# Optimization experiments

Measured on AMD Instinct MI355X. Metric: run time of the kernel, lower is better.

## Reference

```python
import jax, jax.numpy as jnp
import numpy as np

# Emformer config (from torchaudio.models.Emformer in BasicNet4)
D, H, FFN, L = 512, 4, 128, 4      # input_dim, num_heads, ffn_dim, num_layers
SEG, RC = 4, 1                     # segment_length, right_context_length
B, T = 8, 1025
U = T - RC                         # utterance length = 1024
NSEG = -(-U // SEG)                # 256 segments
R = NSEG * RC                      # total right-context frames = 256
DH = D // H


def _right_context_indices():
    # torchaudio _gen_right_context: segment i's right context = frames [(i+1)*SEG : (i+1)*SEG+RC],
    # last block = input[T-RC:]
    idx = [np.arange((i + 1) * SEG, (i + 1) * SEG + RC) for i in range(NSEG - 1)]
    idx.append(np.arange(T - RC, T))
    return np.concatenate(idx)


def _attention_mask():
    # Rows / cols ordered [right-context blocks (seg order), utterance frames].
    # A query belonging to segment i may attend to segment i's right-context block
    # and segment i's utterance frames (left_context_length=0, no memory bank).
    seg_rc = np.repeat(np.arange(NSEG), RC)
    seg_u = np.arange(U) // SEG
    seg_q = np.concatenate([seg_rc, seg_u])
    seg_k = np.concatenate([seg_rc, seg_u])
    return seg_q[:, None] == seg_k[None, :]  # (R+U, R+U), True = allowed


def _ln(x, g, b, eps=1e-5):
    mu = jnp.mean(x, -1, keepdims=True)
    var = jnp.mean(jnp.square(x - mu), -1, keepdims=True)
    return (x - mu) * jax.lax.rsqrt(var + eps) * g + b


def setup_inputs() -> dict:
    key = jax.random.key(0)
    ks = jax.random.split(key, 8)
    s = 0.02
    return {
        "x": jax.random.normal(ks[0], (B, T, D), jnp.float32),
        "Wq": jax.random.normal(ks[1], (L, D, D), jnp.float32) * s,
        "bq": jnp.zeros((L, D), jnp.float32),
        "Wkv": jax.random.normal(ks[2], (L, 2 * D, D), jnp.float32) * s,
        "bkv": jnp.zeros((L, 2 * D), jnp.float32),
        "Wo": jax.random.normal(ks[3], (L, D, D), jnp.float32) * s,
        "bo": jnp.zeros((L, D), jnp.float32),
        "W1": jax.random.normal(ks[4], (L, FFN, D), jnp.float32) * s,
        "b1": jnp.zeros((L, FFN), jnp.float32),
        "W2": jax.random.normal(ks[5], (L, D, FFN), jnp.float32) * s,
        "b2": jnp.zeros((L, D), jnp.float32),
        "ln_in_g": jnp.ones((L, D), jnp.float32),
        "ln_in_b": jnp.zeros((L, D), jnp.float32),
        "ff_ln_g": jnp.ones((L, D), jnp.float32),
        "ff_ln_b": jnp.zeros((L, D), jnp.float32),
        "ln_out_g": jnp.ones((L, D), jnp.float32),
        "ln_out_b": jnp.zeros((L, D), jnp.float32),
    }


def reference(x, Wq, bq, Wkv, bkv, Wo, bo, W1, b1, W2, b2,
              ln_in_g, ln_in_b, ff_ln_g, ff_ln_b, ln_out_g, ln_out_b):
    rc_idx = jnp.asarray(_right_context_indices())
    allowed = jnp.asarray(_attention_mask())
    scale = DH ** -0.5
    u = x[:, :U]          # (B, U, D) utterance
    r = x[:, rc_idx]      # (B, R, D) gathered right-context blocks
    for l in range(L):
        cat = jnp.concatenate([r, u], axis=1)            # (B, R+U, D)
        ln = _ln(cat, ln_in_g[l], ln_in_b[l])            # pre-attention LN
        q = (ln @ Wq[l].T + bq[l]).reshape(B, R + U, H, DH)
        kv = ln @ Wkv[l].T + bkv[l]
        k = kv[..., :D].reshape(B, R + U, H, DH)
        v = kv[..., D:].reshape(B, R + U, H, DH)
        scores = jnp.einsum("bqhd,bkhd->bhqk", q * scale, k)
        scores = jnp.where(allowed, scores, -jnp.inf)
        probs = jax.nn.softmax(scores, axis=-1)
        attn = jnp.einsum("bhqk,bkhd->bqhd", probs, v).reshape(B, R + U, D)
        rc_out = attn @ Wo[l].T + bo[l] + cat            # residual w/ pre-LN input
        h = _ln(rc_out, ff_ln_g[l], ff_ln_b[l])
        h = jax.nn.relu(h @ W1[l].T + b1[l]) @ W2[l].T + b2[l]
        rc_out = _ln(rc_out + h, ln_out_g[l], ln_out_b[l])
        r, u = rc_out[:, :R], rc_out[:, R:]
    return u.mean(axis=1)  # (B, D): mean-pool over utterance frames
```

## Files before the change

### kernel.cpp

```cpp
#include <hip/hip_runtime.h>
#include <cstdint>
#include <cstddef>

#define D_    512
#define H_    4
#define DH_   128
#define FFN_  128
#define L_    4
#define B_    8
#define T_    1025
#define U_    1024
#define NSEG_ 256
#define R_    256
#define TOT_  1280
#define M_    (B_*TOT_)
#define CH_   1536

typedef __attribute__((ext_vector_type(8))) short bf16x8;
typedef __attribute__((ext_vector_type(4))) float f32x4;
typedef unsigned short u16;

__device__ __forceinline__ u16 f2bf(float f) {
  unsigned u = __builtin_bit_cast(unsigned, f);
  u += 0x7fff + ((u >> 16) & 1);
  return (u16)(u >> 16);
}
__device__ __forceinline__ float bf2f(u16 h) {
  unsigned u = ((unsigned)h) << 16;
  return __builtin_bit_cast(float, u);
}

__device__ __forceinline__ void gload_lds16(const void* g, void* l) {
  __builtin_amdgcn_global_load_lds(
      (const __attribute__((address_space(1))) unsigned*)g,
      (__attribute__((address_space(3))) unsigned*)l, 16, 0, 0);
}

__global__ __launch_bounds__(256)
void cvt_all_k(const float* __restrict__ Wq, const float* __restrict__ Wkv,
               const float* __restrict__ Wo, const float* __restrict__ W1,
               const float* __restrict__ W2, const float* __restrict__ bq,
               const float* __restrict__ bkv,
               u16* __restrict__ WQKVb, u16* __restrict__ Wob,
               u16* __restrict__ W1b, u16* __restrict__ W2b,
               float* __restrict__ bQKV) {
  int i4 = blockIdx.x * 256 + threadIdx.x;
  if (i4 < 786432) {
    int e = i4 * 4;
    int l = e / 786432;
    int rem = e - l * 786432;
    int n = rem >> 9, k = rem & 511;
    const float* src = (n < 512) ? (Wq + (size_t)l * 262144 + n * 512 + k)
                                 : (Wkv + (size_t)l * 524288 + (n - 512) * 512 + k);
    float4 v = *(const float4*)src;
    ushort4 o; o.x = f2bf(v.x); o.y = f2bf(v.y); o.z = f2bf(v.z); o.w = f2bf(v.w);
    *(ushort4*)(WQKVb + e) = o;
  } else if (i4 < 1048576) {
    int e = (i4 - 786432) * 4;
    float4 v = *(const float4*)(Wo + e);
    ushort4 o; o.x = f2bf(v.x); o.y = f2bf(v.y); o.z = f2bf(v.z); o.w = f2bf(v.w);
    *(ushort4*)(Wob + e) = o;
  } else if (i4 < 1114112) {
    int e = (i4 - 1048576) * 4;
    float4 v = *(const float4*)(W1 + e);
    ushort4 o; o.x = f2bf(v.x); o.y = f2bf(v.y); o.z = f2bf(v.z); o.w = f2bf(v.w);
    *(ushort4*)(W1b + e) = o;
  } else if (i4 < 1179648) {
    int e = (i4 - 1114112) * 4;
    float4 v = *(const float4*)(W2 + e);
    ushort4 o; o.x = f2bf(v.x); o.y = f2bf(v.y); o.z = f2bf(v.z); o.w = f2bf(v.w);
    *(ushort4*)(W2b + e) = o;
  } else if (i4 < 1181184) {
    int e = (i4 - 1179648) * 4;
    int l = e / 1536, n = e - l * 1536;
#pragma unroll
    for (int t = 0; t < 4; ++t) {
      int nn = n + t;
      bQKV[e + t] = (nn < 512) ? bq[l * 512 + nn] : bkv[l * 1024 + (nn - 512)];
    }
  }
}

__global__ __launch_bounds__(256)
void gather_ln_k(const float* __restrict__ x, const float* __restrict__ g,
                 const float* __restrict__ bb, float* __restrict__ X,
                 u16* __restrict__ LNb) {
  int row = blockIdx.x;
  int tid = threadIdx.x;
  int b = row / TOT_, p = row % TOT_;
  int t = (p < R_) ? ((p < R_ - 1) ? 4 * (p + 1) : (T_ - 1)) : (p - R_);
  const float* xr = x + ((size_t)b * T_ + t) * D_;
  float e0 = xr[tid], e1 = xr[tid + 256];
  X[(size_t)row * D_ + tid] = e0;
  X[(size_t)row * D_ + tid + 256] = e1;
  float s = e0 + e1, ss = e0 * e0 + e1 * e1;
#pragma unroll
  for (int off = 32; off > 0; off >>= 1) {
    s  += __shfl_down(s, off);
    ss += __shfl_down(ss, off);
  }
  __shared__ float red[10];
  int wid = tid >> 6, lane = tid & 63;
  if (lane == 0) { red[wid] = s; red[4 + wid] = ss; }
  __syncthreads();
  if (tid == 0) {
    float S = red[0] + red[1] + red[2] + red[3];
    float SS = red[4] + red[5] + red[6] + red[7];
    float mu = S * (1.0f / D_);
    float var = SS * (1.0f / D_) - mu * mu;
    if (var < 0.f) var = 0.f;
    red[8] = mu; red[9] = rsqrtf(var + 1e-5f);
  }
  __syncthreads();
  float mu = red[8], rs = red[9];
  u16* yr = LNb + (size_t)row * D_;
  yr[tid]       = f2bf((e0 - mu) * rs * g[tid]       + bb[tid]);
  yr[tid + 256] = f2bf((e1 - mu) * rs * g[tid + 256] + bb[tid + 256]);
}

#define GBM 128
#define GBN 128
#define GBK 32

__global__ __launch_bounds__(256)
void gemm_qkv(const u16* __restrict__ A, const u16* __restrict__ Bw,
              const float* __restrict__ bias, u16* __restrict__ Cout,
              int M, int N, int K) {
  __shared__ __align__(16) u16 As[GBM * GBK];
  __shared__ __align__(16) u16 Bs[GBN * GBK];
  const int tid = threadIdx.x;
  const int wid = tid >> 6;
  const int lane = tid & 63;
  const int bm = blockIdx.y * GBM;
  const int bn = blockIdx.x * GBN;
  const int wr = wid >> 1, wc = wid & 1;

  const int srow = tid >> 2;
  const int skoff = (tid & 3) << 3;

  f32x4 acc[4][4] = {};

  const u16* Ag0 = A  + (size_t)(bm + srow)      * K + skoff;
  const u16* Ag1 = A  + (size_t)(bm + 64 + srow) * K + skoff;
  const u16* Bg0 = Bw + (size_t)(bn + srow)      * K + skoff;
  const u16* Bg1 = Bw + (size_t)(bn + 64 + srow) * K + skoff;
  u16* AsW0 = &As[(size_t)(wid * 16)      * GBK];
  u16* AsW1 = &As[(size_t)(64 + wid * 16) * GBK];
  u16* BsW0 = &Bs[(size_t)(wid * 16)      * GBK];
  u16* BsW1 = &Bs[(size_t)(64 + wid * 16) * GBK];

  const int lrow = lane & 15;
  const int lko  = (lane >> 4) * 16;

  for (int k0 = 0; k0 < K; k0 += GBK) {
    __syncthreads();
    gload_lds16(Ag0 + k0, AsW0);
    gload_lds16(Ag1 + k0, AsW1);
    gload_lds16(Bg0 + k0, BsW0);
    gload_lds16(Bg1 + k0, BsW1);
    __syncthreads();

    bf16x8 afrag[4], bfrag[4];
#pragma unroll
    for (int m = 0; m < 4; ++m) {
      int row = wr * 64 + m * 16 + lrow;
      afrag[m] = *(const bf16x8*)((const char*)As + row * (GBK * 2) + lko);
    }
#pragma unroll
    for (int n = 0; n < 4; ++n) {
      int col = wc * 64 + n * 16 + lrow;
      bfrag[n] = *(const bf16x8*)((const char*)Bs + col * (GBK * 2) + lko);
    }
#pragma unroll
    for (int m = 0; m < 4; ++m)
#pragma unroll
      for (int n = 0; n < 4; ++n)
        acc[m][n] = __builtin_amdgcn_mfma_f32_16x16x32_bf16(
            afrag[m], bfrag[n], acc[m][n], 0, 0, 0);
  }

  const int lcol  = lane & 15;
  const int lrow4 = (lane >> 4) * 4;
#pragma unroll
  for (int m = 0; m < 4; ++m) {
    int rowbase = bm + wr * 64 + m * 16 + lrow4;
#pragma unroll
    for (int n = 0; n < 4; ++n) {
      int col = bn + wc * 64 + n * 16 + lcol;
      float bv = bias[col];
#pragma unroll
      for (int j = 0; j < 4; ++j) {
        int row = rowbase + j;
        ((u16*)Cout)[(size_t)row * N + col] = f2bf(acc[m][n][j] + bv);
      }
    }
  }
}

template <int MODE>
__global__ __launch_bounds__(256)
void gemm_row_ln(const u16* __restrict__ A, const u16* __restrict__ Bw,
                 const float* __restrict__ bias, const float* __restrict__ Rsd,
                 float* __restrict__ Xout,
                 const float* __restrict__ g1, const float* __restrict__ b1,
                 const float* __restrict__ g2, const float* __restrict__ b2,
                 u16* __restrict__ OutBf, int K) {
  __shared__ __align__(16) u16 As[32 * 32];
  __shared__ __align__(16) u16 Bs[512 * 32];
  __shared__ float wsum[4][32], wss[4][32], mu_s[32], rs_s[32];
  const int tid = threadIdx.x;
  const int wid = tid >> 6, lane = tid & 63;
  const int bm = blockIdx.x * 32;
  const int l4 = lane >> 2;
  const int k8 = (lane & 3) << 3;
  const int lrow = lane & 15;
  const int lko  = (lane >> 4) * 16;

  f32x4 acc[2][8] = {};

  const u16* Ag = A + (size_t)(bm + (wid & 1) * 16 + l4) * K + k8;

  for (int k0 = 0; k0 < K; k0 += 32) {
    __syncthreads();
    if (wid < 2)
      gload_lds16(Ag + k0, (char*)As + (wid * 16) * 64);
#pragma unroll
    for (int p = 0; p < 8; ++p) {
      int row = wid * 128 + p * 16 + l4;
      gload_lds16(Bw + (size_t)row * K + k0 + k8,
                  (char*)Bs + (wid * 128 + p * 16) * 64);
    }
    __syncthreads();

    bf16x8 af[2], bf[8];
#pragma unroll
    for (int m = 0; m < 2; ++m)
      af[m] = *(const bf16x8*)((const char*)As + (m * 16 + lrow) * 64 + lko);
#pragma unroll
    for (int n = 0; n < 8; ++n)
      bf[n] = *(const bf16x8*)((const char*)Bs + (wid * 128 + n * 16 + lrow) * 64 + lko);
#pragma unroll
    for (int m = 0; m < 2; ++m)
#pragma unroll
      for (int n = 0; n < 8; ++n)
        acc[m][n] = __builtin_amdgcn_mfma_f32_16x16x32_bf16(
            af[m], bf[n], acc[m][n], 0, 0, 0);
  }

  const int lcol = lane & 15;
  const int lr4 = (lane >> 4) * 4;
#pragma unroll
  for (int n = 0; n < 8; ++n) {
    int col = wid * 128 + n * 16 + lcol;
    float bv = bias[col];
#pragma unroll
    for (int m = 0; m < 2; ++m)
#pragma unroll
      for (int j = 0; j < 4; ++j) {
        int row = bm + m * 16 + lr4 + j;
        float t = acc[m][n][j] + bv + Rsd[(size_t)row * D_ + col];
        if (MODE == 0) Xout[(size_t)row * D_ + col] = t;
        acc[m][n][j] = t;
      }
  }

  {
    float s0[2][4] = {}, s1[2][4] = {};
#pragma unroll
    for (int m = 0; m < 2; ++m)
#pragma unroll
      for (int n = 0; n < 8; ++n)
#pragma unroll
        for (int j = 0; j < 4; ++j) {
          float v = acc[m][n][j];
          s0[m][j] += v; s1[m][j] += v * v;
        }
#pragma unroll
    for (int off = 1; off < 16; off <<= 1)
#pragma unroll
      for (int m = 0; m < 2; ++m)
#pragma unroll
        for (int j = 0; j < 4; ++j) {
          s0[m][j] += __shfl_xor(s0[m][j], off);
          s1[m][j] += __shfl_xor(s1[m][j], off);
        }
    if ((lane & 15) == 0) {
#pragma unroll
      for (int m = 0; m < 2; ++m)
#pragma unroll
        for (int j = 0; j < 4; ++j) {
          int r = m * 16 + lr4 + j;
          wsum[wid][r] = s0[m][j]; wss[wid][r] = s1[m][j];
        }
    }
  }
  __syncthreads();
  if (tid < 32) {
    float S  = wsum[0][tid] + wsum[1][tid] + wsum[2][tid] + wsum[3][tid];
    float SS = wss[0][tid] + wss[1][tid] + wss[2][tid] + wss[3][tid];
    float mu = S * (1.0f / D_);
    float var = SS * (1.0f / D_) - mu * mu;
    if (var < 0.f) var = 0.f;
    mu_s[tid] = mu; rs_s[tid] = rsqrtf(var + 1e-5f);
  }
  __syncthreads();

  float gg[8], bv2[8];
#pragma unroll
  for (int n = 0; n < 8; ++n) {
    int col = wid * 128 + n * 16 + lcol;
    gg[n] = g1[col]; bv2[n] = b1[col];
  }
#pragma unroll
  for (int m = 0; m < 2; ++m)
#pragma unroll
    for (int n = 0; n < 8; ++n) {
      int col = wid * 128 + n * 16 + lcol;
#pragma unroll
      for (int j = 0; j < 4; ++j) {
        int r = m * 16 + lr4 + j;
        int row = bm + r;
        float ln = (acc[m][n][j] - mu_s[r]) * rs_s[r] * gg[n] + bv2[n];
        if (MODE == 0) {
          OutBf[(size_t)row * D_ + col] = f2bf(ln);
        } else {
          Xout[(size_t)row * D_ + col] = ln;
          acc[m][n][j] = ln;
        }
      }
    }

  if (MODE == 1) {
    __syncthreads();
    {
      float s0[2][4] = {}, s1[2][4] = {};
#pragma unroll
      for (int m = 0; m < 2; ++m)
#pragma unroll
        for (int n = 0; n < 8; ++n)
#pragma unroll
          for (int j = 0; j < 4; ++j) {
            float v = acc[m][n][j];
            s0[m][j] += v; s1[m][j] += v * v;
          }
#pragma unroll
      for (int off = 1; off < 16; off <<= 1)
#pragma unroll
        for (int m = 0; m < 2; ++m)
#pragma unroll
          for (int j = 0; j < 4; ++j) {
            s0[m][j] += __shfl_xor(s0[m][j], off);
            s1[m][j] += __shfl_xor(s1[m][j], off);
          }
      if ((lane & 15) == 0) {
#pragma unroll
        for (int m = 0; m < 2; ++m)
#pragma unroll
          for (int j = 0; j < 4; ++j) {
            int r = m * 16 + lr4 + j;
            wsum[wid][r] = s0[m][j]; wss[wid][r] = s1[m][j];
          }
      }
    }
    __syncthreads();
    if (tid < 32) {
      float S  = wsum[0][tid] + wsum[1][tid] + wsum[2][tid] + wsum[3][tid];
      float SS = wss[0][tid] + wss[1][tid] + wss[2][tid] + wss[3][tid];
      float mu = S * (1.0f / D_);
      float var = SS * (1.0f / D_) - mu * mu;
      if (var < 0.f) var = 0.f;
      mu_s[tid] = mu; rs_s[tid] = rsqrtf(var + 1e-5f);
    }
    __syncthreads();
#pragma unroll
    for (int n = 0; n < 8; ++n) {
      int col = wid * 128 + n * 16 + lcol;
      gg[n] = g2[col]; bv2[n] = b2[col];
    }
#pragma unroll
    for (int m = 0; m < 2; ++m)
#pragma unroll
      for (int n = 0; n < 8; ++n) {
        int col = wid * 128 + n * 16 + lcol;
#pragma unroll
        for (int j = 0; j < 4; ++j) {
          int r = m * 16 + lr4 + j;
          int row = bm + r;
          float ln = (acc[m][n][j] - mu_s[r]) * rs_s[r] * gg[n] + bv2[n];
          OutBf[(size_t)row * D_ + col] = f2bf(ln);
        }
      }
  }
}

__global__ __launch_bounds__(256)
void gemm_ffn1(const u16* __restrict__ A, const u16* __restrict__ Bw,
               const float* __restrict__ bias, u16* __restrict__ Hout) {
  __shared__ __align__(16) u16 As[32 * 32];
  __shared__ __align__(16) u16 Bs[128 * 32];
  const int tid = threadIdx.x;
  const int wid = tid >> 6, lane = tid & 63;
  const int bm = blockIdx.x * 32;
  const int l4 = lane >> 2;
  const int k8 = (lane & 3) << 3;
  const int lrow = lane & 15;
  const int lko  = (lane >> 4) * 16;

  f32x4 acc[2][2] = {};
  const u16* Ag = A + (size_t)(bm + (wid & 1) * 16 + l4) * D_ + k8;

  for (int k0 = 0; k0 < D_; k0 += 32) {
    __syncthreads();
    if (wid < 2)
      gload_lds16(Ag + k0, (char*)As + (wid * 16) * 64);
#pragma unroll
    for (int p = 0; p < 2; ++p) {
      int row = wid * 32 + p * 16 + l4;
      gload_lds16(Bw + (size_t)row * D_ + k0 + k8,
                  (char*)Bs + (wid * 32 + p * 16) * 64);
    }
    __syncthreads();
    bf16x8 af[2], bf[2];
#pragma unroll
    for (int m = 0; m < 2; ++m)
      af[m] = *(const bf16x8*)((const char*)As + (m * 16 + lrow) * 64 + lko);
#pragma unroll
    for (int n = 0; n < 2; ++n)
      bf[n] = *(const bf16x8*)((const char*)Bs + (wid * 32 + n * 16 + lrow) * 64 + lko);
#pragma unroll
    for (int m = 0; m < 2; ++m)
#pragma unroll
      for (int n = 0; n < 2; ++n)
        acc[m][n] = __builtin_amdgcn_mfma_f32_16x16x32_bf16(
            af[m], bf[n], acc[m][n], 0, 0, 0);
  }

  const int lcol = lane & 15;
  const int lr4 = (lane >> 4) * 4;
#pragma unroll
  for (int m = 0; m < 2; ++m)
#pragma unroll
    for (int n = 0; n < 2; ++n) {
      int col = wid * 32 + n * 16 + lcol;
      float bv = bias[col];
#pragma unroll
      for (int j = 0; j < 4; ++j) {
        int row = bm + m * 16 + lr4 + j;
        float v = fmaxf(acc[m][n][j] + bv, 0.f);
        Hout[(size_t)row * FFN_ + col] = f2bf(v);
      }
    }
}

#define QLD 516
__global__ __launch_bounds__(256)
void attn_k(const u16* __restrict__ QKV, u16* __restrict__ O) {
  int bs = blockIdx.x;
  int b = bs >> 8, s = bs & 255;
  __shared__ float Qs[5][QLD];
  __shared__ float Ks[5][QLD];
  __shared__ float Vs[5][QLD];
  __shared__ float P[H_][5][5];
  int tid = threadIdx.x;
  const float scale = 0.08838834764831845f;
  int rows[5];
  rows[0] = s;
#pragma unroll
  for (int i = 1; i < 5; ++i) rows[i] = R_ + 4 * s + (i - 1);
  for (int idx = tid; idx < 5 * D_; idx += 256) {
    int i = idx >> 9, c = idx & (D_ - 1);
    size_t base = ((size_t)b * TOT_ + rows[i]) * CH_;
    Qs[i][c] = bf2f(QKV[base + c]) * scale;
    Ks[i][c] = bf2f(QKV[base + D_ + c]);
    Vs[i][c] = bf2f(QKV[base + 2 * D_ + c]);
  }
  __syncthreads();
  int h = tid >> 6, lane = tid & 63;
  if (lane < 25) {
    int i = lane / 5, j = lane % 5;
    float sum = 0.f;
    const float* qp = &Qs[i][h * DH_];
    const float* kp = &Ks[j][h * DH_];
#pragma unroll 8
    for (int d = 0; d < DH_; ++d) sum += qp[d] * kp[d];
    P[h][i][j] = sum;
  }
  __syncthreads();
  if (lane < 5) {
    int i = lane;
    float m = P[h][i][0];
#pragma unroll
    for (int j = 1; j < 5; ++j) m = fmaxf(m, P[h][i][j]);
    float e[5], ssum = 0.f;
#pragma unroll
    for (int j = 0; j < 5; ++j) { e[j] = __expf(P[h][i][j] - m); ssum += e[j]; }
    float inv = 1.0f / ssum;
#pragma unroll
    for (int j = 0; j < 5; ++j) P[h][i][j] = e[j] * inv;
  }
  __syncthreads();
  for (int idx = lane; idx < 5 * DH_; idx += 64) {
    int i = idx >> 7, d = idx & (DH_ - 1);
    float o = 0.f;
#pragma unroll
    for (int j = 0; j < 5; ++j) o += P[h][i][j] * Vs[j][h * DH_ + d];
    O[((size_t)b * TOT_ + rows[i]) * D_ + h * DH_ + d] = f2bf(o);
  }
}

__global__ __launch_bounds__(256)
void mean_part_k(const float* __restrict__ X, float* __restrict__ part) {
  int d = blockIdx.x * 256 + threadIdx.x;
  int jc = blockIdx.y;
  int b = blockIdx.z;
  float acc = 0.f;
  const float* base = X + ((size_t)b * TOT_ + R_ + jc * 128) * D_ + d;
  for (int j = 0; j < 128; ++j) acc += base[(size_t)j * D_];
  part[((size_t)b * 8 + jc) * D_ + d] = acc;
}

__global__ __launch_bounds__(256)
void mean_final_k(const float* __restrict__ part, float* __restrict__ out) {
  int i = blockIdx.x * 256 + threadIdx.x;
  int b = i >> 9, d = i & (D_ - 1);
  float acc = 0.f;
#pragma unroll
  for (int c = 0; c < 8; ++c) acc += part[((size_t)b * 8 + c) * D_ + d];
  out[i] = acc * (1.0f / U_);
}

extern "C" void kernel_launch(void* const* d_in, const int* in_sizes, int n_in,
                              void* d_out, int out_size, void* d_ws, size_t ws_size,
                              hipStream_t stream) {
  const float* x      = (const float*)d_in[0];
  const float* Wq     = (const float*)d_in[1];
  const float* bq     = (const float*)d_in[2];
  const float* Wkv    = (const float*)d_in[3];
  const float* bkv    = (const float*)d_in[4];
  const float* Wo     = (const float*)d_in[5];
  const float* bo     = (const float*)d_in[6];
  const float* W1     = (const float*)d_in[7];
  const float* b1     = (const float*)d_in[8];
  const float* W2     = (const float*)d_in[9];
  const float* b2     = (const float*)d_in[10];
  const float* ln_in_g  = (const float*)d_in[11];
  const float* ln_in_b  = (const float*)d_in[12];
  const float* ff_ln_g  = (const float*)d_in[13];
  const float* ff_ln_b  = (const float*)d_in[14];
  const float* ln_out_g = (const float*)d_in[15];
  const float* ln_out_b = (const float*)d_in[16];
  float* out = (float*)d_out;

  char* wsb = (char*)d_ws;
  float* X     = (float*)wsb;
  u16*   LNbuf = (u16*)(wsb + 20971520);
  u16*   QKV   = (u16*)(wsb + 31457280);
  u16*   ATT   = (u16*)(wsb + 62914560);
  u16*   LN2b  = (u16*)(wsb + 73400320);
  u16*   Hb    = (u16*)(wsb + 83886080);
  float* part  = (float*)(wsb + 86507520);
  u16*   WQKVb = (u16*)(wsb + 86638592);
  u16*   Wob   = (u16*)(wsb + 92930048);
  u16*   W1b   = (u16*)(wsb + 95027200);
  u16*   W2b   = (u16*)(wsb + 95551488);
  float* bQKV  = (float*)(wsb + 96075776);

  cvt_all_k<<<4614, 256, 0, stream>>>(Wq, Wkv, Wo, W1, W2, bq, bkv,
                                      WQKVb, Wob, W1b, W2b, bQKV);
  gather_ln_k<<<M_, 256, 0, stream>>>(x, ln_in_g, ln_in_b, X, LNbuf);

  for (int l = 0; l < L_; ++l) {
    const u16* WQKV_l = WQKVb + (size_t)l * CH_ * D_;
    const u16* Wo_l   = Wob   + (size_t)l * D_ * D_;
    const u16* W1_l   = W1b   + (size_t)l * FFN_ * D_;
    const u16* W2_l   = W2b   + (size_t)l * D_ * FFN_;
    const float* bQKV_l = bQKV + (size_t)l * CH_;
    const float* bo_l = bo + (size_t)l * D_;
    const float* b1_l = b1 + (size_t)l * FFN_;
    const float* b2_l = b2 + (size_t)l * D_;

    gemm_qkv<<<dim3(CH_ / GBN, M_ / GBM), 256, 0, stream>>>(
        LNbuf, WQKV_l, bQKV_l, QKV, M_, CH_, D_);

    attn_k<<<B_ * NSEG_, 256, 0, stream>>>(QKV, ATT);

    gemm_row_ln<0><<<M_ / 32, 256, 0, stream>>>(
        ATT, Wo_l, bo_l, X, X,
        ff_ln_g + l * D_, ff_ln_b + l * D_, nullptr, nullptr, LN2b, D_);

    gemm_ffn1<<<M_ / 32, 256, 0, stream>>>(LN2b, W1_l, b1_l, Hb);

    if (l < L_ - 1) {
      gemm_row_ln<1><<<M_ / 32, 256, 0, stream>>>(
          Hb, W2_l, b2_l, X, X,
          ln_out_g + l * D_, ln_out_b + l * D_,
          ln_in_g + (l + 1) * D_, ln_in_b + (l + 1) * D_, LNbuf, FFN_);
    } else {
      gemm_row_ln<2><<<M_ / 32, 256, 0, stream>>>(
          Hb, W2_l, b2_l, X, X,
          ln_out_g + l * D_, ln_out_b + l * D_,
          nullptr, nullptr, nullptr, FFN_);
    }
  }

  mean_part_k<<<dim3(2, 8, 8), 256, 0, stream>>>(X, part);
  mean_final_k<<<(B_ * D_) / 256, 256, 0, stream>>>(part, out);
}
```

Before: 437.7 us.

## Prepack QKV weights in MFMA fragment order and keep full weight slab in LDS

Reorders the QKV weight into a fragment-major layout during the conversion pass. The new QKV GEMM loads a 64-column by full-K weight slab into LDS once per block, then streams A fragments straight from global memory with no per-K-step barriers. This removes the repeated LDS staging and syncs of the old tiled GEMM. In exchange it uses 64KB of LDS per block, reads A without coalescing through LDS, and adds an extra repack kernel.

```diff
diff --git a/kernel.cpp b/kernel.cpp
--- a/kernel.cpp
+++ b/kernel.cpp
@@ -37,41 +37,29 @@
 }
 
 __global__ __launch_bounds__(256)
-void cvt_all_k(const float* __restrict__ Wq, const float* __restrict__ Wkv,
-               const float* __restrict__ Wo, const float* __restrict__ W1,
-               const float* __restrict__ W2, const float* __restrict__ bq,
-               const float* __restrict__ bkv,
-               u16* __restrict__ WQKVb, u16* __restrict__ Wob,
-               u16* __restrict__ W1b, u16* __restrict__ W2b,
-               float* __restrict__ bQKV) {
+void cvt_small_k(const float* __restrict__ Wo, const float* __restrict__ W1,
+                 const float* __restrict__ W2, const float* __restrict__ bq,
+                 const float* __restrict__ bkv,
+                 u16* __restrict__ Wob, u16* __restrict__ W1b,
+                 u16* __restrict__ W2b, float* __restrict__ bQKV) {
   int i4 = blockIdx.x * 256 + threadIdx.x;
-  if (i4 < 786432) {
+  if (i4 < 262144) {
     int e = i4 * 4;
-    int l = e / 786432;
-    int rem = e - l * 786432;
-    int n = rem >> 9, k = rem & 511;
-    const float* src = (n < 512) ? (Wq + (size_t)l * 262144 + n * 512 + k)
-                                 : (Wkv + (size_t)l * 524288 + (n - 512) * 512 + k);
-    float4 v = *(const float4*)src;
-    ushort4 o; o.x = f2bf(v.x); o.y = f2bf(v.y); o.z = f2bf(v.z); o.w = f2bf(v.w);
-    *(ushort4*)(WQKVb + e) = o;
-  } else if (i4 < 1048576) {
-    int e = (i4 - 786432) * 4;
     float4 v = *(const float4*)(Wo + e);
     ushort4 o; o.x = f2bf(v.x); o.y = f2bf(v.y); o.z = f2bf(v.z); o.w = f2bf(v.w);
     *(ushort4*)(Wob + e) = o;
-  } else if (i4 < 1114112) {
-    int e = (i4 - 1048576) * 4;
+  } else if (i4 < 327680) {
+    int e = (i4 - 262144) * 4;
     float4 v = *(const float4*)(W1 + e);
     ushort4 o; o.x = f2bf(v.x); o.y = f2bf(v.y); o.z = f2bf(v.z); o.w = f2bf(v.w);
     *(ushort4*)(W1b + e) = o;
-  } else if (i4 < 1179648) {
-    int e = (i4 - 1114112) * 4;
+  } else if (i4 < 393216) {
+    int e = (i4 - 327680) * 4;
     float4 v = *(const float4*)(W2 + e);
     ushort4 o; o.x = f2bf(v.x); o.y = f2bf(v.y); o.z = f2bf(v.z); o.w = f2bf(v.w);
     *(ushort4*)(W2b + e) = o;
-  } else if (i4 < 1181184) {
-    int e = (i4 - 1179648) * 4;
+  } else if (i4 < 394752) {
+    int e = (i4 - 393216) * 4;
     int l = e / 1536, n = e - l * 1536;
 #pragma unroll
     for (int t = 0; t < 4; ++t) {
@@ -79,6 +67,30 @@
       bQKV[e + t] = (nn < 512) ? bq[l * 512 + nn] : bkv[l * 1024 + (nn - 512)];
     }
   }
+}
+
+__global__ __launch_bounds__(256)
+void repack_qkv_k(const float* __restrict__ Wq, const float* __restrict__ Wkv,
+                  u16* __restrict__ Wpack) {
+  int g = blockIdx.x * 256 + threadIdx.x;
+  int lane = g & 63;
+  int nf = (g >> 6) & 3;
+  int ks = (g >> 8) & 15;
+  int nb = (g >> 12) % 24;
+  int l  = g >> 12; l /= 24;
+  int col = nb * 64 + nf * 16 + (lane & 15);
+  int k   = ks * 32 + (lane >> 4) * 8;
+  const float* src = (col < 512)
+      ? (Wq  + (size_t)l * 262144 + (size_t)col * 512 + k)
+      : (Wkv + (size_t)l * 524288 + (size_t)(col - 512) * 512 + k);
+  float4 v0 = *(const float4*)(src);
+  float4 v1 = *(const float4*)(src + 4);
+  ushort4 o0, o1;
+  o0.x = f2bf(v0.x); o0.y = f2bf(v0.y); o0.z = f2bf(v0.z); o0.w = f2bf(v0.w);
+  o1.x = f2bf(v1.x); o1.y = f2bf(v1.y); o1.z = f2bf(v1.z); o1.w = f2bf(v1.w);
+  u16* dst = Wpack + (size_t)g * 8;
+  *(ushort4*)(dst)     = o0;
+  *(ushort4*)(dst + 4) = o1;
 }
 
 __global__ __launch_bounds__(256)
@@ -118,81 +130,59 @@
   yr[tid + 256] = f2bf((e1 - mu) * rs * g[tid + 256] + bb[tid + 256]);
 }
 
-#define GBM 128
-#define GBN 128
-#define GBK 32
-
-__global__ __launch_bounds__(256)
-void gemm_qkv(const u16* __restrict__ A, const u16* __restrict__ Bw,
-              const float* __restrict__ bias, u16* __restrict__ Cout,
-              int M, int N, int K) {
-  __shared__ __align__(16) u16 As[GBM * GBK];
-  __shared__ __align__(16) u16 Bs[GBN * GBK];
+__global__ __launch_bounds__(512, 4)
+void gemm_qkv_ws(const u16* __restrict__ A, const u16* __restrict__ Wpack_l,
+                 const float* __restrict__ bias, u16* __restrict__ Cout) {
+  __shared__ __align__(16) u16 Wlds[32768];
   const int tid = threadIdx.x;
   const int wid = tid >> 6;
   const int lane = tid & 63;
-  const int bm = blockIdx.y * GBM;
-  const int bn = blockIdx.x * GBN;
-  const int wr = wid >> 1, wc = wid & 1;
-
-  const int srow = tid >> 2;
-  const int skoff = (tid & 3) << 3;
+  const int bn = blockIdx.x * 64;
+  const int bm = blockIdx.y * 512;
+
+  const u16* Wsrc = Wpack_l + (size_t)blockIdx.x * 32768;
+#pragma unroll
+  for (int r = 0; r < 8; ++r) {
+    int idx16 = r * 512 + wid * 64;
+    gload_lds16(Wsrc + (size_t)(idx16 + lane) * 8, Wlds + (size_t)idx16 * 8);
+  }
 
   f32x4 acc[4][4] = {};
 
-  const u16* Ag0 = A  + (size_t)(bm + srow)      * K + skoff;
-  const u16* Ag1 = A  + (size_t)(bm + 64 + srow) * K + skoff;
-  const u16* Bg0 = Bw + (size_t)(bn + srow)      * K + skoff;
-  const u16* Bg1 = Bw + (size_t)(bn + 64 + srow) * K + skoff;
-  u16* AsW0 = &As[(size_t)(wid * 16)      * GBK];
-  u16* AsW1 = &As[(size_t)(64 + wid * 16) * GBK];
-  u16* BsW0 = &Bs[(size_t)(wid * 16)      * GBK];
-  u16* BsW1 = &Bs[(size_t)(64 + wid * 16) * GBK];
-
-  const int lrow = lane & 15;
-  const int lko  = (lane >> 4) * 16;
-
-  for (int k0 = 0; k0 < K; k0 += GBK) {
-    __syncthreads();
-    gload_lds16(Ag0 + k0, AsW0);
-    gload_lds16(Ag1 + k0, AsW1);
-    gload_lds16(Bg0 + k0, BsW0);
-    gload_lds16(Bg1 + k0, BsW1);
-    __syncthreads();
-
-    bf16x8 afrag[4], bfrag[4];
-#pragma unroll
-    for (int m = 0; m < 4; ++m) {
-      int row = wr * 64 + m * 16 + lrow;
-      afrag[m] = *(const bf16x8*)((const char*)As + row * (GBK * 2) + lko);
-    }
-#pragma unroll
-    for (int n = 0; n < 4; ++n) {
-      int col = wc * 64 + n * 16 + lrow;
-      bfrag[n] = *(const bf16x8*)((const char*)Bs + col * (GBK * 2) + lko);
-    }
+  const u16* Arow = A + (size_t)(bm + wid * 64 + (lane & 15)) * D_ + ((lane >> 4) << 3);
+
+  __syncthreads();
+
+#pragma unroll
+  for (int ks = 0; ks < 16; ++ks) {
+    bf16x8 af[4];
 #pragma unroll
     for (int m = 0; m < 4; ++m)
-#pragma unroll
-      for (int n = 0; n < 4; ++n)
-        acc[m][n] = __builtin_amdgcn_mfma_f32_16x16x32_bf16(
-            afrag[m], bfrag[n], acc[m][n], 0, 0, 0);
-  }
-
-  const int lcol  = lane & 15;
-  const int lrow4 = (lane >> 4) * 4;
+      af[m] = *(const bf16x8*)(Arow + (size_t)(m * 16) * D_ + ks * 32);
+#pragma unroll
+    for (int nf = 0; nf < 4; ++nf) {
+      bf16x8 bf = *(const bf16x8*)(Wlds + (size_t)((ks * 4 + nf) * 64 + lane) * 8);
+#pragma unroll
+      for (int m = 0; m < 4; ++m)
+        acc[m][nf] = __builtin_amdgcn_mfma_f32_16x16x32_bf16(
+            af[m], bf, acc[m][nf], 0, 0, 0);
+    }
+  }
+
+  const int lcol = lane & 15;
+  const int lr4 = (lane >> 4) * 4;
+  float bv[4];
+#pragma unroll
+  for (int nf = 0; nf < 4; ++nf) bv[nf] = bias[bn + nf * 16 + lcol];
 #pragma unroll
   for (int m = 0; m < 4; ++m) {
-    int rowbase = bm + wr * 64 + m * 16 + lrow4;
-#pragma unroll
-    for (int n = 0; n < 4; ++n) {
-      int col = bn + wc * 64 + n * 16 + lcol;
-      float bv = bias[col];
-#pragma unroll
-      for (int j = 0; j < 4; ++j) {
-        int row = rowbase + j;
-        ((u16*)Cout)[(size_t)row * N + col] = f2bf(acc[m][n][j] + bv);
-      }
+    int rowbase = bm + wid * 64 + m * 16 + lr4;
+#pragma unroll
+    for (int nf = 0; nf < 4; ++nf) {
+      int col = bn + nf * 16 + lcol;
+#pragma unroll
+      for (int j = 0; j < 4; ++j)
+        Cout[(size_t)(rowbase + j) * CH_ + col] = f2bf(acc[m][nf][j] + bv[nf]);
     }
   }
 }
@@ -559,18 +549,19 @@
   u16*   LN2b  = (u16*)(wsb + 73400320);
   u16*   Hb    = (u16*)(wsb + 83886080);
   float* part  = (float*)(wsb + 86507520);
-  u16*   WQKVb = (u16*)(wsb + 86638592);
+  u16*   Wpack = (u16*)(wsb + 86638592);
   u16*   Wob   = (u16*)(wsb + 92930048);
   u16*   W1b   = (u16*)(wsb + 95027200);
   u16*   W2b   = (u16*)(wsb + 95551488);
   float* bQKV  = (float*)(wsb + 96075776);
 
-  cvt_all_k<<<4614, 256, 0, stream>>>(Wq, Wkv, Wo, W1, W2, bq, bkv,
-                                      WQKVb, Wob, W1b, W2b, bQKV);
+  cvt_small_k<<<1542, 256, 0, stream>>>(Wo, W1, W2, bq, bkv,
+                                        Wob, W1b, W2b, bQKV);
+  repack_qkv_k<<<1536, 256, 0, stream>>>(Wq, Wkv, Wpack);
   gather_ln_k<<<M_, 256, 0, stream>>>(x, ln_in_g, ln_in_b, X, LNbuf);
 
   for (int l = 0; l < L_; ++l) {
-    const u16* WQKV_l = WQKVb + (size_t)l * CH_ * D_;
+    const u16* Wpack_l = Wpack + (size_t)l * 24 * 32768;
     const u16* Wo_l   = Wob   + (size_t)l * D_ * D_;
     const u16* W1_l   = W1b   + (size_t)l * FFN_ * D_;
     const u16* W2_l   = W2b   + (size_t)l * D_ * FFN_;
@@ -579,8 +570,7 @@
     const float* b1_l = b1 + (size_t)l * FFN_;
     const float* b2_l = b2 + (size_t)l * D_;
 
-    gemm_qkv<<<dim3(CH_ / GBN, M_ / GBM), 256, 0, stream>>>(
-        LNbuf, WQKV_l, bQKV_l, QKV, M_, CH_, D_);
+    gemm_qkv_ws<<<dim3(24, 20), 512, 0, stream>>>(LNbuf, Wpack_l, bQKV_l, QKV);
 
     attn_k<<<B_ * NSEG_, 256, 0, stream>>>(QKV, ATT);
 
```

After: 460.7 us. 1.05x slower.

## Fuse output projection, FFN layernorm and FFN1 into one kernel; remap QKV blocks

Applied to the files above, without the earlier changes.

The output-projection GEMM with residual and feed-forward layernorm is merged with the first FFN GEMM. The normalized tile stays in swizzled shared memory, so the bf16 LN2 buffer no longer makes a global round trip and one launch per layer is removed. The QKV GEMM now uses a 1D grid whose block index is remapped so that row blocks are grouped by XCD, which should improve L2 reuse. The attention loader switches to 16-byte vector loads. The fused kernel uses about 67KB of shared memory, which may lower occupancy.

```diff
diff --git a/kernel.cpp b/kernel.cpp
--- a/kernel.cpp
+++ b/kernel.cpp
@@ -118,21 +118,23 @@
   yr[tid + 256] = f2bf((e1 - mu) * rs * g[tid + 256] + bb[tid + 256]);
 }
 
-#define GBM 128
-#define GBN 128
 #define GBK 32
 
 __global__ __launch_bounds__(256)
 void gemm_qkv(const u16* __restrict__ A, const u16* __restrict__ Bw,
-              const float* __restrict__ bias, u16* __restrict__ Cout,
-              int M, int N, int K) {
-  __shared__ __align__(16) u16 As[GBM * GBK];
-  __shared__ __align__(16) u16 Bs[GBN * GBK];
+              const float* __restrict__ bias, u16* __restrict__ Cout) {
+  __shared__ __align__(16) u16 As[128 * GBK];
+  __shared__ __align__(16) u16 Bs[128 * GBK];
   const int tid = threadIdx.x;
   const int wid = tid >> 6;
   const int lane = tid & 63;
-  const int bm = blockIdx.y * GBM;
-  const int bn = blockIdx.x * GBN;
+  const int bid = blockIdx.x;
+  const int xcd = bid & 7;
+  const int t = bid >> 3;
+  const int cb = t % 12;
+  const int rb = xcd * 10 + t / 12;
+  const int bm = rb * 128;
+  const int bn = cb * 128;
   const int wr = wid >> 1, wc = wid & 1;
 
   const int srow = tid >> 2;
@@ -140,10 +142,10 @@
 
   f32x4 acc[4][4] = {};
 
-  const u16* Ag0 = A  + (size_t)(bm + srow)      * K + skoff;
-  const u16* Ag1 = A  + (size_t)(bm + 64 + srow) * K + skoff;
-  const u16* Bg0 = Bw + (size_t)(bn + srow)      * K + skoff;
-  const u16* Bg1 = Bw + (size_t)(bn + 64 + srow) * K + skoff;
+  const u16* Ag0 = A  + (size_t)(bm + srow)      * D_ + skoff;
+  const u16* Ag1 = A  + (size_t)(bm + 64 + srow) * D_ + skoff;
+  const u16* Bg0 = Bw + (size_t)(bn + srow)      * D_ + skoff;
+  const u16* Bg1 = Bw + (size_t)(bn + 64 + srow) * D_ + skoff;
   u16* AsW0 = &As[(size_t)(wid * 16)      * GBK];
   u16* AsW1 = &As[(size_t)(64 + wid * 16) * GBK];
   u16* BsW0 = &Bs[(size_t)(wid * 16)      * GBK];
@@ -152,7 +154,7 @@
   const int lrow = lane & 15;
   const int lko  = (lane >> 4) * 16;
 
-  for (int k0 = 0; k0 < K; k0 += GBK) {
+  for (int k0 = 0; k0 < D_; k0 += GBK) {
     __syncthreads();
     gload_lds16(Ag0 + k0, AsW0);
     gload_lds16(Ag1 + k0, AsW1);
@@ -191,10 +193,178 @@
 #pragma unroll
       for (int j = 0; j < 4; ++j) {
         int row = rowbase + j;
-        ((u16*)Cout)[(size_t)row * N + col] = f2bf(acc[m][n][j] + bv);
+        Cout[(size_t)row * CH_ + col] = f2bf(acc[m][n][j] + bv);
       }
     }
   }
+}
+
+__global__ __launch_bounds__(256)
+void gemm_oproj_ffn1(const u16* __restrict__ ATT, const u16* __restrict__ Wo_l,
+                     const float* __restrict__ bo, const float* __restrict__ Rsd,
+                     float* __restrict__ Xout,
+                     const float* __restrict__ gff, const float* __restrict__ bff,
+                     const u16* __restrict__ W1_l, const float* __restrict__ b1,
+                     u16* __restrict__ Hout) {
+  __shared__ __align__(16) u16 As[32 * 32];
+  __shared__ __align__(16) u16 Bs[512 * 32];
+  __shared__ __align__(16) u16 LN2[32 * 512];
+  __shared__ float wsum[4][32], wss[4][32], mu_s[32], rs_s[32];
+  const int tid = threadIdx.x;
+  const int wid = tid >> 6, lane = tid & 63;
+  const int bm = blockIdx.x * 32;
+  const int l4 = lane >> 2;
+  const int k8 = (lane & 3) << 3;
+  const int lrow = lane & 15;
+  const int lko  = (lane >> 4) * 16;
+
+  f32x4 acc[2][8] = {};
+
+  const u16* Ag = ATT + (size_t)(bm + (wid & 1) * 16 + l4) * D_ + k8;
+
+  for (int k0 = 0; k0 < D_; k0 += 32) {
+    __syncthreads();
+    if (wid < 2)
+      gload_lds16(Ag + k0, (char*)As + (wid * 16) * 64);
+#pragma unroll
+    for (int p = 0; p < 8; ++p) {
+      int row = wid * 128 + p * 16 + l4;
+      gload_lds16(Wo_l + (size_t)row * D_ + k0 + k8,
+                  (char*)Bs + (wid * 128 + p * 16) * 64);
+    }
+    __syncthreads();
+
+    bf16x8 af[2], bf[8];
+#pragma unroll
+    for (int m = 0; m < 2; ++m)
+      af[m] = *(const bf16x8*)((const char*)As + (m * 16 + lrow) * 64 + lko);
+#pragma unroll
+    for (int n = 0; n < 8; ++n)
+      bf[n] = *(const bf16x8*)((const char*)Bs + (wid * 128 + n * 16 + lrow) * 64 + lko);
+#pragma unroll
+    for (int m = 0; m < 2; ++m)
+#pragma unroll
+      for (int n = 0; n < 8; ++n)
+        acc[m][n] = __builtin_amdgcn_mfma_f32_16x16x32_bf16(
+            af[m], bf[n], acc[m][n], 0, 0, 0);
+  }
+
+  const int lcol = lane & 15;
+  const int lr4 = (lane >> 4) * 4;
+#pragma unroll
+  for (int n = 0; n < 8; ++n) {
+    int col = wid * 128 + n * 16 + lcol;
+    float bv = bo[col];
+#pragma unroll
+    for (int m = 0; m < 2; ++m)
+#pragma unroll
+      for (int j = 0; j < 4; ++j) {
+        int row = bm + m * 16 + lr4 + j;
+        float t = acc[m][n][j] + bv + Rsd[(size_t)row * D_ + col];
+        Xout[(size_t)row * D_ + col] = t;
+        acc[m][n][j] = t;
+      }
+  }
+
+  {
+    float s0[2][4] = {}, s1[2][4] = {};
+#pragma unroll
+    for (int m = 0; m < 2; ++m)
+#pragma unroll
+      for (int n = 0; n < 8; ++n)
+#pragma unroll
+        for (int j = 0; j < 4; ++j) {
+          float v = acc[m][n][j];
+          s0[m][j] += v; s1[m][j] += v * v;
+        }
+#pragma unroll
+    for (int off = 1; off < 16; off <<= 1)
+#pragma unroll
+      for (int m = 0; m < 2; ++m)
+#pragma unroll
+        for (int j = 0; j < 4; ++j) {
+          s0[m][j] += __shfl_xor(s0[m][j], off);
+          s1[m][j] += __shfl_xor(s1[m][j], off);
+        }
+    if ((lane & 15) == 0) {
+#pragma unroll
+      for (int m = 0; m < 2; ++m)
+#pragma unroll
+        for (int j = 0; j < 4; ++j) {
+          int r = m * 16 + lr4 + j;
+          wsum[wid][r] = s0[m][j]; wss[wid][r] = s1[m][j];
+        }
+    }
+  }
+  __syncthreads();
+  if (tid < 32) {
+    float S  = wsum[0][tid] + wsum[1][tid] + wsum[2][tid] + wsum[3][tid];
+    float SS = wss[0][tid] + wss[1][tid] + wss[2][tid] + wss[3][tid];
+    float mu = S * (1.0f / D_);
+    float var = SS * (1.0f / D_) - mu * mu;
+    if (var < 0.f) var = 0.f;
+    mu_s[tid] = mu; rs_s[tid] = rsqrtf(var + 1e-5f);
+  }
+  __syncthreads();
+
+#pragma unroll
+  for (int n = 0; n < 8; ++n) {
+    int col = wid * 128 + n * 16 + lcol;
+    float gg = gff[col], bb = bff[col];
+#pragma unroll
+    for (int m = 0; m < 2; ++m)
+#pragma unroll
+      for (int j = 0; j < 4; ++j) {
+        int r = m * 16 + lr4 + j;
+        float ln = (acc[m][n][j] - mu_s[r]) * rs_s[r] * gg + bb;
+        int byteoff = (r * 1024 + col * 2) ^ ((r & 7) << 4);
+        *(u16*)((char*)LN2 + byteoff) = f2bf(ln);
+      }
+  }
+
+  f32x4 acc2[2][2] = {};
+  for (int k0 = 0; k0 < D_; k0 += 32) {
+    __syncthreads();
+#pragma unroll
+    for (int p = 0; p < 2; ++p) {
+      int cbase = p * 256 + wid * 64;
+      int chunk = cbase + lane;
+      gload_lds16(W1_l + (size_t)(chunk >> 2) * D_ + k0 + ((chunk & 3) << 3),
+                  (char*)Bs + (size_t)cbase * 16);
+    }
+    __syncthreads();
+
+    bf16x8 af[2], bf[2];
+#pragma unroll
+    for (int m = 0; m < 2; ++m) {
+      int row = m * 16 + lrow;
+      int byteoff = (row * 1024 + k0 * 2 + lko) ^ ((row & 7) << 4);
+      af[m] = *(const bf16x8*)((const char*)LN2 + byteoff);
+    }
+#pragma unroll
+    for (int n = 0; n < 2; ++n)
+      bf[n] = *(const bf16x8*)((const char*)Bs + (wid * 32 + n * 16 + lrow) * 64 + lko);
+#pragma unroll
+    for (int m = 0; m < 2; ++m)
+#pragma unroll
+      for (int n = 0; n < 2; ++n)
+        acc2[m][n] = __builtin_amdgcn_mfma_f32_16x16x32_bf16(
+            af[m], bf[n], acc2[m][n], 0, 0, 0);
+  }
+
+#pragma unroll
+  for (int m = 0; m < 2; ++m)
+#pragma unroll
+    for (int n = 0; n < 2; ++n) {
+      int col = wid * 32 + n * 16 + lcol;
+      float bv = b1[col];
+#pragma unroll
+      for (int j = 0; j < 4; ++j) {
+        int row = bm + m * 16 + lr4 + j;
+        float v = fmaxf(acc2[m][n][j] + bv, 0.f);
+        Hout[(size_t)row * FFN_ + col] = f2bf(v);
+      }
+    }
 }
 
 template <int MODE>
@@ -259,7 +429,6 @@
       for (int j = 0; j < 4; ++j) {
         int row = bm + m * 16 + lr4 + j;
         float t = acc[m][n][j] + bv + Rsd[(size_t)row * D_ + col];
-        if (MODE == 0) Xout[(size_t)row * D_ + col] = t;
         acc[m][n][j] = t;
       }
   }
@@ -321,12 +490,8 @@
         int r = m * 16 + lr4 + j;
         int row = bm + r;
         float ln = (acc[m][n][j] - mu_s[r]) * rs_s[r] * gg[n] + bv2[n];
-        if (MODE == 0) {
-          OutBf[(size_t)row * D_ + col] = f2bf(ln);
-        } else {
-          Xout[(size_t)row * D_ + col] = ln;
-          acc[m][n][j] = ln;
-        }
+        Xout[(size_t)row * D_ + col] = ln;
+        acc[m][n][j] = ln;
       }
     }
 
@@ -391,65 +556,6 @@
         }
       }
   }
-}
-
-__global__ __launch_bounds__(256)
-void gemm_ffn1(const u16* __restrict__ A, const u16* __restrict__ Bw,
-               const float* __restrict__ bias, u16* __restrict__ Hout) {
-  __shared__ __align__(16) u16 As[32 * 32];
-  __shared__ __align__(16) u16 Bs[128 * 32];
-  const int tid = threadIdx.x;
-  const int wid = tid >> 6, lane = tid & 63;
-  const int bm = blockIdx.x * 32;
-  const int l4 = lane >> 2;
-  const int k8 = (lane & 3) << 3;
-  const int lrow = lane & 15;
-  const int lko  = (lane >> 4) * 16;
-
-  f32x4 acc[2][2] = {};
-  const u16* Ag = A + (size_t)(bm + (wid & 1) * 16 + l4) * D_ + k8;
-
-  for (int k0 = 0; k0 < D_; k0 += 32) {
-    __syncthreads();
-    if (wid < 2)
-      gload_lds16(Ag + k0, (char*)As + (wid * 16) * 64);
-#pragma unroll
-    for (int p = 0; p < 2; ++p) {
-      int row = wid * 32 + p * 16 + l4;
-      gload_lds16(Bw + (size_t)row * D_ + k0 + k8,
-                  (char*)Bs + (wid * 32 + p * 16) * 64);
-    }
-    __syncthreads();
-    bf16x8 af[2], bf[2];
-#pragma unroll
-    for (int m = 0; m < 2; ++m)
-      af[m] = *(const bf16x8*)((const char*)As + (m * 16 + lrow) * 64 + lko);
-#pragma unroll
-    for (int n = 0; n < 2; ++n)
-      bf[n] = *(const bf16x8*)((const char*)Bs + (wid * 32 + n * 16 + lrow) * 64 + lko);
-#pragma unroll
-    for (int m = 0; m < 2; ++m)
-#pragma unroll
-      for (int n = 0; n < 2; ++n)
-        acc[m][n] = __builtin_amdgcn_mfma_f32_16x16x32_bf16(
-            af[m], bf[n], acc[m][n], 0, 0, 0);
-  }
-
-  const int lcol = lane & 15;
-  const int lr4 = (lane >> 4) * 4;
-#pragma unroll
-  for (int m = 0; m < 2; ++m)
-#pragma unroll
-    for (int n = 0; n < 2; ++n) {
-      int col = wid * 32 + n * 16 + lcol;
-      float bv = bias[col];
-#pragma unroll
-      for (int j = 0; j < 4; ++j) {
-        int row = bm + m * 16 + lr4 + j;
-        float v = fmaxf(acc[m][n][j] + bv, 0.f);
-        Hout[(size_t)row * FFN_ + col] = f2bf(v);
-      }
-    }
 }
 
 #define QLD 516
@@ -467,12 +573,20 @@
   rows[0] = s;
 #pragma unroll
   for (int i = 1; i < 5; ++i) rows[i] = R_ + 4 * s + (i - 1);
-  for (int idx = tid; idx < 5 * D_; idx += 256) {
-    int i = idx >> 9, c = idx & (D_ - 1);
-    size_t base = ((size_t)b * TOT_ + rows[i]) * CH_;
-    Qs[i][c] = bf2f(QKV[base + c]) * scale;
-    Ks[i][c] = bf2f(QKV[base + D_ + c]);
-    Vs[i][c] = bf2f(QKV[base + 2 * D_ + c]);
+  for (int idx = tid; idx < 960; idx += 256) {
+    int mtx = idx / 320;
+    int rem = idx - mtx * 320;
+    int i = rem >> 6, c8 = rem & 63;
+    size_t base = ((size_t)b * TOT_ + rows[i]) * CH_ + mtx * 512 + c8 * 8;
+    bf16x8 v = *(const bf16x8*)(QKV + base);
+    float* dst = (mtx == 0) ? &Qs[i][c8 * 8] : (mtx == 1 ? &Ks[i][c8 * 8] : &Vs[i][c8 * 8]);
+    if (mtx == 0) {
+#pragma unroll
+      for (int t = 0; t < 8; ++t) dst[t] = bf2f((u16)v[t]) * scale;
+    } else {
+#pragma unroll
+      for (int t = 0; t < 8; ++t) dst[t] = bf2f((u16)v[t]);
+    }
   }
   __syncthreads();
   int h = tid >> 6, lane = tid & 63;
@@ -556,7 +670,6 @@
   u16*   LNbuf = (u16*)(wsb + 20971520);
   u16*   QKV   = (u16*)(wsb + 31457280);
   u16*   ATT   = (u16*)(wsb + 62914560);
-  u16*   LN2b  = (u16*)(wsb + 73400320);
   u16*   Hb    = (u16*)(wsb + 83886080);
   float* part  = (float*)(wsb + 86507520);
   u16*   WQKVb = (u16*)(wsb + 86638592);
@@ -579,16 +692,13 @@
     const float* b1_l = b1 + (size_t)l * FFN_;
     const float* b2_l = b2 + (size_t)l * D_;
 
-    gemm_qkv<<<dim3(CH_ / GBN, M_ / GBM), 256, 0, stream>>>(
-        LNbuf, WQKV_l, bQKV_l, QKV, M_, CH_, D_);
+    gemm_qkv<<<960, 256, 0, stream>>>(LNbuf, WQKV_l, bQKV_l, QKV);
 
     attn_k<<<B_ * NSEG_, 256, 0, stream>>>(QKV, ATT);
 
-    gemm_row_ln<0><<<M_ / 32, 256, 0, stream>>>(
+    gemm_oproj_ffn1<<<M_ / 32, 256, 0, stream>>>(
         ATT, Wo_l, bo_l, X, X,
-        ff_ln_g + l * D_, ff_ln_b + l * D_, nullptr, nullptr, LN2b, D_);
-
-    gemm_ffn1<<<M_ / 32, 256, 0, stream>>>(LN2b, W1_l, b1_l, Hb);
+        ff_ln_g + l * D_, ff_ln_b + l * D_, W1_l, b1_l, Hb);
 
     if (l < L_ - 1) {
       gemm_row_ln<1><<<M_ / 32, 256, 0, stream>>>(
```

After: 474.0 us. +8.3%, slower.
